# Kernel optimization log

Hardware: AMD Instinct MI355X
Metric: run time of the kernel (lower is better)

## Reference

```python
import jax, jax.numpy as jnp
import numpy as np

TOKENS, IN_F, OUT_F = 16, 4096, 11008


def setup_inputs() -> dict:
    key = jax.random.key(0)
    k1, k2, k3, k4 = jax.random.split(key, 4)
    x = jax.random.normal(k1, (TOKENS, IN_F), dtype=jnp.float32)
    weight_int8 = jax.random.randint(k2, (OUT_F, IN_F), 0, 127, dtype=jnp.int32)
    # per-row scale, clamped >= 1e-8 as in the torch module
    scale = jnp.maximum(jax.random.uniform(k3, (OUT_F, 1), dtype=jnp.float32) * 0.02, 1e-8)
    bias = jax.random.normal(k4, (OUT_F,), dtype=jnp.float32)
    return {"x": x, "weight_int8": weight_int8, "scale": scale, "bias": bias}


def reference(x, weight_int8, scale, bias):
    # dequantize: [out, in] fp32 weight, cast to activation dtype
    w = (weight_int8.astype(jnp.float32) * scale).astype(x.dtype)
    # F.linear: x @ w.T + bias
    return jnp.einsum('ti,oi->to', x, w) + bias.astype(x.dtype)
```

## Files before the change

kernel.cpp:

```cpp
#include <hip/hip_runtime.h>
#include <hip/hip_bf16.h>

typedef float f32x4 __attribute__((ext_vector_type(4)));
typedef short short8 __attribute__((ext_vector_type(8)));

constexpr int IN_F    = 4096;
constexpr int OUT_F   = 11008;
constexpr int NTILES  = OUT_F / 16;
constexpr int CHUNK_K = 256;
constexpr int NCHUNK  = IN_F / CHUNK_K;
constexpr int ROWW    = 260;
constexpr int WAVES   = 4;

#define GLBP(p) ((const __attribute__((address_space(1))) void*)(p))
#define LDSP(p) ((__attribute__((address_space(3))) void*)(p))

__device__ __forceinline__ unsigned short bf16_rne(float f) {
    unsigned u = __builtin_bit_cast(unsigned, f);
    u += 0x7fffu + ((u >> 16) & 1u);
    return (unsigned short)(u >> 16);
}
__device__ __forceinline__ short bf16_from_int(int v) {
    float f = (float)v;
    return (short)(__builtin_bit_cast(unsigned, f) >> 16);
}

__global__ __launch_bounds__(256) void cvt_x_kernel(
    const float* __restrict__ x, unsigned short* __restrict__ xb)
{
    const int i = (blockIdx.x * 256 + threadIdx.x) * 4;
    float4 v = *(const float4*)(x + i);
    ushort4 o;
    o.x = bf16_rne(v.x); o.y = bf16_rne(v.y);
    o.z = bf16_rne(v.z); o.w = bf16_rne(v.w);
    *(ushort4*)(xb + i) = o;
}

__global__ __launch_bounds__(256, 4) void Int8Linear_kernel(
    const unsigned short* __restrict__ xb,
    const int*   __restrict__ w,
    const float* __restrict__ scale,
    const float* __restrict__ bias,
    float*       __restrict__ out)
{
    __shared__ uint32_t lds[2 * 16 * ROWW];

    const int tid  = threadIdx.x;
    const int wave = tid >> 6;
    const int lane = tid & 63;
    const int m    = lane & 15;
    const int g    = lane >> 4;
    const int n0   = blockIdx.x * 16;

    auto stage = [&](int c) {
        const int buf = (c & 1) * 16 * ROWW;
        #pragma unroll
        for (int r = 0; r < 4; ++r) {
            const int row = wave * 4 + r;
            const int* gp = w + (size_t)(n0 + row) * IN_F + c * CHUNK_K + lane * 4;
            uint32_t*  lp = (uint32_t*)&lds[buf + row * ROWW + lane * 4];
            __builtin_amdgcn_global_load_lds(
                (const __attribute__((address_space(1))) uint32_t*)gp,
                (__attribute__((address_space(3))) uint32_t*)lp, 16, 0, 0);
        }
    };

    f32x4 acc = {0.f, 0.f, 0.f, 0.f};
    stage(0);

    for (int c = 0; c < NCHUNK; ++c) {
        __syncthreads();
        if (c + 1 < NCHUNK) stage(c + 1);

        const int buf = (c & 1) * 16 * ROWW;
        #pragma unroll
        for (int s = 0; s < 2; ++s) {
            const int kc = (wave * 2 + s) * 32;
            const int k0 = c * CHUNK_K + kc;

            short8 a = *(const short8*)(xb + (size_t)m * IN_F + k0 + g * 8);

            const uint32_t* bw = &lds[buf + m * ROWW + kc + g * 8];
            int4 wa = *(const int4*)bw;
            int4 wb = *(const int4*)(bw + 4);

            short8 b;
            b[0] = bf16_from_int(wa.x); b[1] = bf16_from_int(wa.y);
            b[2] = bf16_from_int(wa.z); b[3] = bf16_from_int(wa.w);
            b[4] = bf16_from_int(wb.x); b[5] = bf16_from_int(wb.y);
            b[6] = bf16_from_int(wb.z); b[7] = bf16_from_int(wb.w);

            acc = __builtin_amdgcn_mfma_f32_16x16x32_bf16(a, b, acc, 0, 0, 0);
        }
    }

    __syncthreads();
    float* red = (float*)lds;
    #pragma unroll
    for (int r = 0; r < 4; ++r)
        red[(wave * 16 + g * 4 + r) * 16 + m] = acc[r];
    __syncthreads();

    const int row = tid >> 4;
    const int col = tid & 15;
    float s = 0.f;
    #pragma unroll
    for (int v = 0; v < WAVES; ++v)
        s += red[(v * 16 + row) * 16 + col];
    const int o = n0 + col;
    out[(size_t)row * OUT_F + o] = s * scale[o] + bias[o];
}

extern "C" void kernel_launch(void* const* d_in, const int* in_sizes, int n_in,
                              void* d_out, int out_size, void* d_ws, size_t ws_size,
                              hipStream_t stream) {
    const float* x     = (const float*)d_in[0];
    const int*   w     = (const int*)d_in[1];
    const float* scale = (const float*)d_in[2];
    const float* bias  = (const float*)d_in[3];
    float*       out   = (float*)d_out;
    unsigned short* xb = (unsigned short*)d_ws;

    cvt_x_kernel<<<64, 256, 0, stream>>>(x, xb);
    Int8Linear_kernel<<<NTILES, 256, 0, stream>>>(xb, w, scale, bias, out);
}
```

Before: 45.58 us.

## Triple-buffer weight staging with explicit vmcnt waits and preload x into registers

Weight chunks now go through a three-deep LDS ring. Two chunks are prefetched before the loop, and each wave waits with a manual s_waitcnt vmcnt before a bare s_barrier, replacing the __syncthreads-then-stage pattern. All activation fragments for the whole K range are loaded into registers once, up front, instead of being re-read from global memory every chunk, and the loop is fully unrolled. The aim is to keep more weight bytes in flight and take global x loads off the critical path. The cost is much higher register and LDS use, which lowers occupancy (launch bounds go from 4 to 3 blocks per SM) and depends on exact vmcnt accounting.

```diff
diff --git a/kernel.cpp b/kernel.cpp
--- a/kernel.cpp
+++ b/kernel.cpp
@@ -10,10 +10,8 @@
 constexpr int CHUNK_K = 256;
 constexpr int NCHUNK  = IN_F / CHUNK_K;
 constexpr int ROWW    = 260;
+constexpr int NBUF    = 3;
 constexpr int WAVES   = 4;
-
-#define GLBP(p) ((const __attribute__((address_space(1))) void*)(p))
-#define LDSP(p) ((__attribute__((address_space(3))) void*)(p))
 
 __device__ __forceinline__ unsigned short bf16_rne(float f) {
     unsigned u = __builtin_bit_cast(unsigned, f);
@@ -36,14 +34,14 @@
     *(ushort4*)(xb + i) = o;
 }
 
-__global__ __launch_bounds__(256, 4) void Int8Linear_kernel(
+__global__ __launch_bounds__(256, 3) void Int8Linear_kernel(
     const unsigned short* __restrict__ xb,
     const int*   __restrict__ w,
     const float* __restrict__ scale,
     const float* __restrict__ bias,
     float*       __restrict__ out)
 {
-    __shared__ uint32_t lds[2 * 16 * ROWW];
+    __shared__ uint32_t lds[NBUF * 16 * ROWW];
 
     const int tid  = threadIdx.x;
     const int wave = tid >> 6;
@@ -52,34 +50,46 @@
     const int g    = lane >> 4;
     const int n0   = blockIdx.x * 16;
 
+    short8 xf[NCHUNK][2];
+    #pragma unroll
+    for (int c = 0; c < NCHUNK; ++c) {
+        #pragma unroll
+        for (int s = 0; s < 2; ++s) {
+            const int k0 = c * CHUNK_K + (wave * 2 + s) * 32;
+            xf[c][s] = *(const short8*)(xb + (size_t)m * IN_F + k0 + g * 8);
+        }
+    }
+
     auto stage = [&](int c) {
-        const int buf = (c & 1) * 16 * ROWW;
+        const int buf = (c % NBUF) * 16 * ROWW;
         #pragma unroll
         for (int r = 0; r < 4; ++r) {
             const int row = wave * 4 + r;
             const int* gp = w + (size_t)(n0 + row) * IN_F + c * CHUNK_K + lane * 4;
-            uint32_t*  lp = (uint32_t*)&lds[buf + row * ROWW + lane * 4];
             __builtin_amdgcn_global_load_lds(
                 (const __attribute__((address_space(1))) uint32_t*)gp,
-                (__attribute__((address_space(3))) uint32_t*)lp, 16, 0, 0);
+                (__attribute__((address_space(3))) uint32_t*)&lds[buf + row * ROWW + lane * 4],
+                16, 0, 0);
         }
     };
 
     f32x4 acc = {0.f, 0.f, 0.f, 0.f};
+
     stage(0);
+    stage(1);
+    asm volatile("s_waitcnt vmcnt(8)" ::: "memory");
 
+    #pragma unroll
     for (int c = 0; c < NCHUNK; ++c) {
-        __syncthreads();
-        if (c + 1 < NCHUNK) stage(c + 1);
+        if (c < NCHUNK - 1) asm volatile("s_waitcnt vmcnt(4)" ::: "memory");
+        else                asm volatile("s_waitcnt vmcnt(0)" ::: "memory");
+        __builtin_amdgcn_s_barrier();
+        asm volatile("" ::: "memory");
 
-        const int buf = (c & 1) * 16 * ROWW;
+        const int buf = (c % NBUF) * 16 * ROWW;
         #pragma unroll
         for (int s = 0; s < 2; ++s) {
             const int kc = (wave * 2 + s) * 32;
-            const int k0 = c * CHUNK_K + kc;
-
-            short8 a = *(const short8*)(xb + (size_t)m * IN_F + k0 + g * 8);
-
             const uint32_t* bw = &lds[buf + m * ROWW + kc + g * 8];
             int4 wa = *(const int4*)bw;
             int4 wb = *(const int4*)(bw + 4);
@@ -90,8 +100,10 @@
             b[4] = bf16_from_int(wb.x); b[5] = bf16_from_int(wb.y);
             b[6] = bf16_from_int(wb.z); b[7] = bf16_from_int(wb.w);
 
-            acc = __builtin_amdgcn_mfma_f32_16x16x32_bf16(a, b, acc, 0, 0, 0);
+            acc = __builtin_amdgcn_mfma_f32_16x16x32_bf16(xf[c][s], b, acc, 0, 0, 0);
         }
+
+        if (c + 2 < NCHUNK) stage(c + 2);
     }
 
     __syncthreads();
```

Result: slower. 47.86 us (+5.0%).
